# Performance work log

Hardware: AMD Instinct MI355X
Metric: run time of the kernel (lower is better)

The kernel has to match this reference:

```python
import jax, jax.numpy as jnp
import numpy as np

B, S, D, H = 2, 2048, 1024, 16
DK = D // H

def setup_inputs() -> dict:
    key = jax.random.key(0)
    ks = jax.random.split(key, 12)
    scale = 1.0 / np.sqrt(D)
    return {
        "q": jax.random.normal(ks[0], (B, S, D), jnp.float32),
        "k": jax.random.normal(ks[1], (B, S, D), jnp.float32),
        "v": jax.random.normal(ks[2], (B, S, D), jnp.float32),
        "mask": jax.random.randint(ks[3], (B, 1, S, S), 0, 2, jnp.int32),
        "w_q": jax.random.normal(ks[4], (D, D), jnp.float32) * scale,
        "b_q": jnp.zeros((D,), jnp.float32),
        "w_k": jax.random.normal(ks[5], (D, D), jnp.float32) * scale,
        "b_k": jnp.zeros((D,), jnp.float32),
        "w_v": jax.random.normal(ks[6], (D, D), jnp.float32) * scale,
        "b_v": jnp.zeros((D,), jnp.float32),
        "w_o": jax.random.normal(ks[7], (D, D), jnp.float32) * scale,
        "b_o": jnp.zeros((D,), jnp.float32),
    }

def reference(q, k, v, mask, w_q, b_q, w_k, b_k, w_v, b_v, w_o, b_o):
    # projections (nn.Linear: x @ W^T + b)
    Q = q @ w_q.T + b_q  # [B,S,D]
    K = k @ w_k.T + b_k
    V = v @ w_v.T + b_v
    # split heads -> [B,H,S,DK]
    Q = Q.reshape(B, S, H, DK).transpose(0, 2, 1, 3)
    K = K.reshape(B, S, H, DK).transpose(0, 2, 1, 3)
    V = V.reshape(B, S, H, DK).transpose(0, 2, 1, 3)
    scores = jnp.einsum("bhqd,bhkd->bhqk", Q, K) / jnp.sqrt(jnp.float32(DK))
    scores = jnp.where(mask == 0, jnp.float32(-1e9), scores)
    attn = jax.nn.softmax(scores, axis=-1)  # dropout p=0 -> identity
    x = jnp.einsum("bhqk,bhkd->bhqd", attn, V)
    x = x.transpose(0, 2, 1, 3).reshape(B, S, D)
    return x @ w_o.T + b_o
```

## Files before the change

kernel.cpp:

```cpp
#include <hip/hip_runtime.h>
#include <hip/hip_bf16.h>
#include <cstdint>
#include <cstddef>

typedef short bf16x8 __attribute__((ext_vector_type(8)));
typedef short bf16x4v __attribute__((ext_vector_type(4)));
typedef float f32x4 __attribute__((ext_vector_type(4)));
typedef unsigned int uint32x2 __attribute__((ext_vector_type(2)));
typedef __hip_bfloat16 bf16;

constexpr int Bb = 2, Ss = 2048, Dd = 1024, Hh = 16, DKk = 64;

__device__ __forceinline__ void async_lds16(void* lds, const void* g) {
  __builtin_amdgcn_global_load_lds(
      (const __attribute__((address_space(1))) void*)g,
      (__attribute__((address_space(3))) void*)lds, 16, 0, 0);
}

__device__ __forceinline__ float bf2f(bf16 x) { return __bfloat162float(x); }
__device__ __forceinline__ short f2bf(float x) {
  bf16 h = __float2bfloat16(x);
  return *(short*)&h;
}
__device__ __forceinline__ short f2bf_fast(float x) {
  return (short)((__float_as_uint(x) + 0x8000u) >> 16);
}
__device__ __forceinline__ float bfs2f(short s) {
  return __uint_as_float(((uint32_t)(uint16_t)s) << 16);
}
__device__ __forceinline__ uint32_t cvtpk_bf16(float lo, float hi) {
  uint32_t r;
  asm("v_cvt_pk_bf16_f32 %0, %1, %2" : "=v"(r) : "v"(lo), "v"(hi));
  return r;
}
__device__ __forceinline__ uint32x2 pl32swap(uint32_t d, uint32_t s) {
  return __builtin_amdgcn_permlane32_swap(d, s, false, false);
}
__device__ __forceinline__ uint32x2 pl16swap(uint32_t d, uint32_t s) {
  return __builtin_amdgcn_permlane16_swap(d, s, false, false);
}

struct CvtArgs {
  const float* src[12];
  short* dst[12];
  int n[12];
  int count;
};

__global__ __launch_bounds__(256)
void cvt_all(CvtArgs a, const int* __restrict__ mask, uint32_t* __restrict__ bits)
{
  const int t = blockIdx.y;
  if (t == 11) {
    const int stride = 1024 * 256;
    int i = blockIdx.x * 256 + threadIdx.x;
#pragma unroll 4
    for (int it = 0; it < 32; ++it, i += stride) {
      const unsigned long long bal = __ballot(mask[i] != 0);
      if ((threadIdx.x & 63) == 0)
        *(unsigned long long*)(bits + (i >> 5)) = bal;
    }
    return;
  }
  if (t >= a.count) return;
  const float* s = a.src[t];
  short* d = a.dst[t];
  const int n = a.n[t];
  const int stride = gridDim.x * blockDim.x * 4;
  for (int i = (blockIdx.x * blockDim.x + threadIdx.x) * 4; i < n; i += stride) {
    const float4 v = *(const float4*)(s + i);
    bf16x4v o;
    o[0] = f2bf(v.x); o[1] = f2bf(v.y); o[2] = f2bf(v.z); o[3] = f2bf(v.w);
    *(bf16x4v*)(d + i) = o;
  }
}

__global__ __launch_bounds__(256, 3)
void gemm_bt(const bf16* __restrict__ A0, const bf16* __restrict__ A1, const bf16* __restrict__ A2,
             const bf16* __restrict__ W0, const bf16* __restrict__ W1, const bf16* __restrict__ W2,
             const bf16* __restrict__ b0, const bf16* __restrict__ b1, const bf16* __restrict__ b2,
             void* __restrict__ O0, void* __restrict__ O1, void* __restrict__ O2,
             float scale0, int vtrans)
{
  extern __shared__ char smem[];
  const int mt  = blockIdx.x;
  const int by  = blockIdx.y;
  const int mat = by >> 3;
  const int nt  = by & 7;
  const bf16* A    = (mat == 0) ? A0 : (mat == 1) ? A1 : A2;
  const bf16* W    = (mat == 0) ? W0 : (mat == 1) ? W1 : W2;
  const bf16* bias = (mat == 0) ? b0 : (mat == 1) ? b1 : b2;
  void*       Out  = (mat == 0) ? O0 : (mat == 1) ? O1 : O2;
  const float scale = (mat == 0) ? scale0 : 1.0f;

  const int tid  = threadIdx.x;
  const int w    = tid >> 6;
  const int lane = tid & 63;
  const int quad = lane >> 4;
  const int l16  = lane & 15;
  const int wm   = (w & 1) * 64;
  const int wn   = (w >> 1) * 64;

  const int srow = lane >> 3;
  const int sseg = (lane & 7) ^ srow;

  const char* Abytes = (const char*)A;
  const char* Wbytes = (const char*)W;

  f32x4 acc[4][4];
#pragma unroll
  for (int i = 0; i < 4; ++i)
#pragma unroll
    for (int j = 0; j < 4; ++j) acc[i][j] = f32x4{0.f, 0.f, 0.f, 0.f};

  for (int kt = 0; kt < 16; ++kt) {
    __syncthreads();
#pragma unroll
    for (int c = 0; c < 4; ++c) {
      const int r0 = w * 32 + c * 8;
      async_lds16(smem + r0 * 128,
                  Abytes + (size_t)(mt * 128 + r0 + srow) * 2048 + kt * 128 + sseg * 16);
      async_lds16(smem + 16384 + r0 * 128,
                  Wbytes + (size_t)(nt * 128 + r0 + srow) * 2048 + kt * 128 + sseg * 16);
    }
    __syncthreads();
#pragma unroll
    for (int s = 0; s < 2; ++s) {
      bf16x8 af[4], bfg[4];
#pragma unroll
      for (int mb = 0; mb < 4; ++mb) {
        const int row = wm + mb * 16 + l16;
        af[mb] = *(const bf16x8*)(smem + row * 128 + (((4 * s + quad) ^ (row & 7)) * 16));
      }
#pragma unroll
      for (int nb = 0; nb < 4; ++nb) {
        const int row = wn + nb * 16 + l16;
        bfg[nb] = *(const bf16x8*)(smem + 16384 + row * 128 + (((4 * s + quad) ^ (row & 7)) * 16));
      }
#pragma unroll
      for (int mb = 0; mb < 4; ++mb)
#pragma unroll
        for (int nb = 0; nb < 4; ++nb)
          acc[mb][nb] = __builtin_amdgcn_mfma_f32_16x16x32_bf16(af[mb], bfg[nb], acc[mb][nb], 0, 0, 0);
    }
  }

  if (vtrans && mat == 2) {
    __syncthreads();
#pragma unroll
    for (int nb = 0; nb < 4; ++nb) {
      const int dk = wn + nb * 16 + l16;
      const float bv = bf2f(bias[nt * 128 + dk]);
#pragma unroll
      for (int mb = 0; mb < 4; ++mb) {
        const int s0 = wm + mb * 16 + quad * 4;
        bf16x4v pk;
#pragma unroll
        for (int r = 0; r < 4; ++r) pk[r] = f2bf_fast(acc[mb][nb][r] + bv);
        *(bf16x4v*)(smem + dk * 256 + (((s0 >> 3) ^ (dk & 15)) * 16) + (s0 & 7) * 2) = pk;
      }
    }
    __syncthreads();
    const int bidx  = (mt * 128) >> 11;
    const int sbase = (mt * 128) & 2047;
#pragma unroll
    for (int i = 0; i < 8; ++i) {
      const int dk  = i * 16 + (tid >> 4);
      const int seg = tid & 15;
      bf16x8 vrow = *(const bf16x8*)(smem + dk * 256 + ((seg ^ (dk & 15)) * 16));
      *(bf16x8*)((bf16*)Out + (size_t)bidx * 2097152 + (size_t)(nt * 128 + dk) * 2048
                 + sbase + seg * 8) = vrow;
    }
  } else {
#pragma unroll
    for (int nb = 0; nb < 4; ++nb) {
      const int col = nt * 128 + wn + nb * 16 + l16;
      const float bv = bf2f(bias[col]);
#pragma unroll
      for (int mb = 0; mb < 4; ++mb) {
#pragma unroll
        for (int r = 0; r < 4; ++r) {
          const int row = mt * 128 + wm + mb * 16 + quad * 4 + r;
          short s = f2bf_fast((acc[mb][nb][r] + bv) * scale);
          ((short*)Out)[(size_t)row * 1024 + col] = s;
        }
      }
    }
  }
}

__global__ __launch_bounds__(256, 4)
void gemm_out(const bf16* __restrict__ A, const bf16* __restrict__ W,
              const bf16* __restrict__ bias, float* __restrict__ Out)
{
  __shared__ char smem[16384];
  const int mt = blockIdx.x;
  const int nt = blockIdx.y;
  const int tid = threadIdx.x, w = tid >> 6, lane = tid & 63;
  const int quad = lane >> 4, l16 = lane & 15;
  const int wm = (w & 1) * 32, wn = (w >> 1) * 32;
  const int srow = lane >> 3;
  const int sseg = (lane & 7) ^ (srow & 7);

  const char* Abytes = (const char*)A;
  const char* Wbytes = (const char*)W;

  f32x4 acc[2][2];
#pragma unroll
  for (int i = 0; i < 2; ++i)
#pragma unroll
    for (int j = 0; j < 2; ++j) acc[i][j] = f32x4{0.f, 0.f, 0.f, 0.f};

  for (int kt = 0; kt < 16; ++kt) {
    __syncthreads();
#pragma unroll
    for (int c = 0; c < 2; ++c) {
      const int r0 = c * 32 + w * 8;
      async_lds16(smem + c * 4096 + w * 1024,
                  Abytes + (size_t)(mt * 64 + r0 + srow) * 2048 + kt * 128 + sseg * 16);
      async_lds16(smem + 8192 + c * 4096 + w * 1024,
                  Wbytes + (size_t)(nt * 64 + r0 + srow) * 2048 + kt * 128 + sseg * 16);
    }
    __syncthreads();
#pragma unroll
    for (int s = 0; s < 2; ++s) {
      bf16x8 af[2], bfg[2];
#pragma unroll
      for (int mb = 0; mb < 2; ++mb) {
        const int row = wm + mb * 16 + l16;
        af[mb] = *(const bf16x8*)(smem + row * 128 + (((4 * s + quad) ^ (row & 7)) * 16));
      }
#pragma unroll
      for (int nb = 0; nb < 2; ++nb) {
        const int row = wn + nb * 16 + l16;
        bfg[nb] = *(const bf16x8*)(smem + 8192 + row * 128 + (((4 * s + quad) ^ (row & 7)) * 16));
      }
#pragma unroll
      for (int mb = 0; mb < 2; ++mb)
#pragma unroll
        for (int nb = 0; nb < 2; ++nb)
          acc[mb][nb] = __builtin_amdgcn_mfma_f32_16x16x32_bf16(af[mb], bfg[nb], acc[mb][nb], 0, 0, 0);
    }
  }

#pragma unroll
  for (int nb = 0; nb < 2; ++nb) {
    const int col = nt * 64 + wn + nb * 16 + l16;
    const float bv = bf2f(bias[col]);
#pragma unroll
    for (int mb = 0; mb < 2; ++mb) {
#pragma unroll
      for (int r = 0; r < 4; ++r) {
        const int row = mt * 64 + wm + mb * 16 + quad * 4 + r;
        Out[(size_t)row * 1024 + col] = acc[mb][nb][r] + bv;
      }
    }
  }
}

__device__ __forceinline__ void stage_kv(char* KbB, char* VtB,
    const bf16* __restrict__ Kp, const bf16* __restrict__ VpT,
    size_t headoff, size_t vbase, int kb, int w, int lane)
{
#pragma unroll
  for (int c = 0; c < 2; ++c) {
    const int rowK = c * 32 + w * 8 + (lane >> 3);
    const int segK = (lane & 7) ^ (rowK & 7);
    async_lds16(KbB + c * 4096 + w * 1024,
                Kp + headoff + (size_t)(kb + rowK) * Dd + segK * 8);
    const int rowV = c * 32 + w * 8 + (lane >> 3);
    const int segV = (lane & 7) ^ (rowV & 7);
    async_lds16(VtB + c * 4096 + w * 1024,
                VpT + vbase + (size_t)rowV * 2048 + kb + segV * 8);
  }
}

__global__ __launch_bounds__(256, 4)
void attn(const bf16* __restrict__ Qp, const bf16* __restrict__ Kp,
          const bf16* __restrict__ VpT, const uint32_t* __restrict__ mbits,
          bf16* __restrict__ Opart, float* __restrict__ Lpart)
{
  __shared__ char smem[16384];
  char* Kb = smem;
  char* Vt = smem + 8192;

  const int tile  = blockIdx.x;
  const int split = blockIdx.y;
  const int qt = tile & 15, h = (tile >> 4) & 15, b = tile >> 8;
  const int tid = threadIdx.x, w = tid >> 6, lane = tid & 63;
  const int quad = lane >> 4, l16 = lane & 15;
  const int qb = qt * 128;
  const size_t headoff = (size_t)b * (Ss * Dd) + h * DKk;
  const size_t vbase = (size_t)b * 2097152 + (size_t)h * 131072;

  const int kc0 = (split == 0) ? 0 : (split == 1) ? 11 : 22;
  const int kc1 = (split == 0) ? 11 : (split == 1) ? 22 : 32;

  bf16x8 qf[2][2];
#pragma unroll
  for (int set = 0; set < 2; ++set)
#pragma unroll
    for (int s2 = 0; s2 < 2; ++s2) {
      const int row = qb + w * 32 + set * 16 + l16;
      qf[set][s2] = *(const bf16x8*)(Qp + headoff + (size_t)row * Dd + s2 * 32 + quad * 8);
    }

  bf16x8 onesv;
#pragma unroll
  for (int j = 0; j < 8; ++j) onesv[j] = (short)0x3F80;

  f32x4 o[2][4];
  f32x4 oL[2];
#pragma unroll
  for (int set = 0; set < 2; ++set) {
    oL[set] = f32x4{0.f, 0.f, 0.f, 0.f};
#pragma unroll
    for (int nbk = 0; nbk < 4; ++nbk) o[set][nbk] = f32x4{0.f, 0.f, 0.f, 0.f};
  }

  const uint32_t* mrow0 = mbits + (size_t)(b * Ss + qb + w * 32 + l16) * 64;
  const uint32_t* mrow1 = mrow0 + 16 * 64;

  for (int kc = kc0; kc < kc1; ++kc) {
    const int kb = kc * 64;
    const uint2 mwv0 = *(const uint2*)(mrow0 + kc * 2);
    const uint2 mwv1 = *(const uint2*)(mrow1 + kc * 2);
    __syncthreads();
    stage_kv(Kb, Vt, Kp, VpT, headoff, vbase, kb, w, lane);
    __syncthreads();

    const uint32_t mw0[2] = {mwv0.x, mwv0.y};
    const uint32_t mw1[2] = {mwv1.x, mwv1.y};

#pragma unroll
    for (int sl = 0; sl < 2; ++sl) {
      f32x4 sc[2][2];
#pragma unroll
      for (int set = 0; set < 2; ++set)
#pragma unroll
        for (int nbh = 0; nbh < 2; ++nbh) sc[set][nbh] = f32x4{0.f, 0.f, 0.f, 0.f};
      __builtin_amdgcn_s_setprio(1);
#pragma unroll
      for (int s2 = 0; s2 < 2; ++s2)
#pragma unroll
        for (int nbh = 0; nbh < 2; ++nbh) {
          const int row = (sl * 2 + nbh) * 16 + l16;
          bf16x8 kf = *(const bf16x8*)(Kb + row * 128 + (((s2 * 4 + quad) ^ (row & 7)) * 16));
          sc[0][nbh] = __builtin_amdgcn_mfma_f32_16x16x32_bf16(kf, qf[0][s2], sc[0][nbh], 0, 0, 0);
          sc[1][nbh] = __builtin_amdgcn_mfma_f32_16x16x32_bf16(kf, qf[1][s2], sc[1][nbh], 0, 0, 0);
        }
      __builtin_amdgcn_s_setprio(0);

      bf16x8 pf[2];
#pragma unroll
      for (int set = 0; set < 2; ++set) {
        const uint32_t mword = (set == 0) ? mw0[sl] : mw1[sl];
        uint32_t pk[2][2];
#pragma unroll
        for (int nbh = 0; nbh < 2; ++nbh) {
          const uint32_t nib = (mword >> (nbh * 16 + quad * 4)) & 0xFu;
          const float e0 = __builtin_amdgcn_exp2f(sc[set][nbh][0]);
          const float e1 = __builtin_amdgcn_exp2f(sc[set][nbh][1]);
          const float e2 = __builtin_amdgcn_exp2f(sc[set][nbh][2]);
          const float e3 = __builtin_amdgcn_exp2f(sc[set][nbh][3]);
          const float p0 = (nib & 1u) ? e0 : 0.f;
          const float p1 = (nib & 2u) ? e1 : 0.f;
          const float p2 = (nib & 4u) ? e2 : 0.f;
          const float p3 = (nib & 8u) ? e3 : 0.f;
          pk[nbh][0] = cvtpk_bf16(p0, p1);
          pk[nbh][1] = cvtpk_bf16(p2, p3);
        }
        const uint32x2 r0 = pl32swap(pk[0][0], pk[1][0]);
        const uint32x2 r1 = pl32swap(pk[0][1], pk[1][1]);
        const uint32x2 t0 = pl16swap(r0.x, r0.y);
        const uint32x2 t1 = pl16swap(r1.x, r1.y);
        union { uint32_t u[4]; bf16x8 v; } U;
        U.u[0] = t0.x; U.u[1] = t1.x; U.u[2] = t0.y; U.u[3] = t1.y;
        pf[set] = U.v;
      }

      __builtin_amdgcn_s_setprio(1);
      oL[0] = __builtin_amdgcn_mfma_f32_16x16x32_bf16(pf[0], onesv, oL[0], 0, 0, 0);
      oL[1] = __builtin_amdgcn_mfma_f32_16x16x32_bf16(pf[1], onesv, oL[1], 0, 0, 0);
#pragma unroll
      for (int nbk = 0; nbk < 4; ++nbk) {
        const int row = nbk * 16 + l16;
        bf16x8 vf = *(const bf16x8*)(Vt + row * 128 + (((sl * 4 + quad) ^ (row & 7)) * 16));
        o[0][nbk] = __builtin_amdgcn_mfma_f32_16x16x32_bf16(pf[0], vf, o[0][nbk], 0, 0, 0);
        o[1][nbk] = __builtin_amdgcn_mfma_f32_16x16x32_bf16(pf[1], vf, o[1][nbk], 0, 0, 0);
      }
      __builtin_amdgcn_s_setprio(0);
    }
  }

#pragma unroll
  for (int set = 0; set < 2; ++set) {
    const int rbase = tile * 128 + w * 32 + set * 16;
#pragma unroll
    for (int r = 0; r < 4; ++r) {
      const int rglob = rbase + quad * 4 + r;
#pragma unroll
      for (int nbk = 0; nbk < 4; ++nbk) {
        short s = f2bf_fast(o[set][nbk][r]);
        ((short*)Opart)[((size_t)split * 65536 + rglob) * 64 + nbk * 16 + l16] = s;
      }
    }
    if (l16 == 0) {
#pragma unroll
      for (int r = 0; r < 4; ++r)
        Lpart[(size_t)split * 65536 + rbase + quad * 4 + r] = oL[set][r];
    }
  }
}

__global__ __launch_bounds__(256)
void combine(const bf16* __restrict__ Opart, const float* __restrict__ Lpart,
             bf16* __restrict__ Xa)
{
  const int t = threadIdx.x;
  const int row = blockIdx.x * 32 + (t >> 3);
  const int dkc = (t & 7) * 8;
  const float L = Lpart[row] + Lpart[65536 + row] + Lpart[131072 + row];
  const float inv = 1.0f / L;
  const bf16x8 O0 = *(const bf16x8*)(Opart + (size_t)row * 64 + dkc);
  const bf16x8 O1 = *(const bf16x8*)(Opart + ((size_t)65536 + row) * 64 + dkc);
  const bf16x8 O2 = *(const bf16x8*)(Opart + ((size_t)131072 + row) * 64 + dkc);
  bf16x8 res;
#pragma unroll
  for (int j = 0; j < 8; ++j)
    res[j] = f2bf_fast((bfs2f(O0[j]) + bfs2f(O1[j]) + bfs2f(O2[j])) * inv);
  const int tile = row >> 7, qlocal = row & 127;
  const int b = tile >> 8, h = (tile >> 4) & 15, q = (tile & 15) * 128 + qlocal;
  *(bf16x8*)(Xa + (size_t)(b * 2048 + q) * 1024 + h * 64 + dkc) = res;
}

extern "C" void kernel_launch(void* const* d_in, const int* in_sizes, int n_in,
                              void* d_out, int out_size, void* d_ws, size_t ws_size,
                              hipStream_t stream)
{
  const float* q  = (const float*)d_in[0];
  const float* k  = (const float*)d_in[1];
  const float* v  = (const float*)d_in[2];
  const int*   mk = (const int*)d_in[3];
  const float* wq = (const float*)d_in[4];
  const float* bq = (const float*)d_in[5];
  const float* wk = (const float*)d_in[6];
  const float* bk = (const float*)d_in[7];
  const float* wv = (const float*)d_in[8];
  const float* bv = (const float*)d_in[9];
  const float* wo = (const float*)d_in[10];
  const float* bo = (const float*)d_in[11];
  float* out = (float*)d_out;

  char* ws = (char*)d_ws;
  bf16* qb_  = (bf16*)(ws + ((size_t)0  << 20));
  bf16* kb_  = (bf16*)(ws + ((size_t)8  << 20));
  bf16* vb_  = (bf16*)(ws + ((size_t)16 << 20));
  bf16* Qp   = (bf16*)(ws + ((size_t)24 << 20));
  bf16* Kp   = (bf16*)(ws + ((size_t)32 << 20));
  bf16* VpT  = (bf16*)(ws + ((size_t)40 << 20));
  bf16* wqb  = (bf16*)(ws + ((size_t)48 << 20));
  bf16* wkb  = (bf16*)(ws + ((size_t)50 << 20));
  bf16* wvb  = (bf16*)(ws + ((size_t)52 << 20));
  bf16* wob  = (bf16*)(ws + ((size_t)54 << 20));
  bf16* bqb  = (bf16*)(ws + ((size_t)56 << 20));
  bf16* bkb  = (bf16*)(ws + ((size_t)56 << 20) + 2048);
  bf16* bvb  = (bf16*)(ws + ((size_t)56 << 20) + 4096);
  bf16* bob  = (bf16*)(ws + ((size_t)56 << 20) + 6144);
  uint32_t* mbits = (uint32_t*)(ws + ((size_t)56 << 20) + 65536);
  bf16*  Opart = (bf16*)(ws + ((size_t)0 << 20));
  float* Lpart = (float*)(ws + ((size_t)48 << 20));
  bf16*  Xa    = (bf16*)(ws + ((size_t)24 << 20));

  const int NA = Bb * Ss * Dd;
  const int NW = Dd * Dd;

  CvtArgs ca;
  ca.src[0] = q;  ca.dst[0] = (short*)qb_; ca.n[0] = NA;
  ca.src[1] = k;  ca.dst[1] = (short*)kb_; ca.n[1] = NA;
  ca.src[2] = v;  ca.dst[2] = (short*)vb_; ca.n[2] = NA;
  ca.src[3] = wq; ca.dst[3] = (short*)wqb; ca.n[3] = NW;
  ca.src[4] = wk; ca.dst[4] = (short*)wkb; ca.n[4] = NW;
  ca.src[5] = wv; ca.dst[5] = (short*)wvb; ca.n[5] = NW;
  ca.src[6] = wo; ca.dst[6] = (short*)wob; ca.n[6] = NW;
  ca.src[7] = bq; ca.dst[7] = (short*)bqb; ca.n[7] = Dd;
  ca.src[8] = bk; ca.dst[8] = (short*)bkb; ca.n[8] = Dd;
  ca.src[9] = bv; ca.dst[9] = (short*)bvb; ca.n[9] = Dd;
  ca.src[10] = bo; ca.dst[10] = (short*)bob; ca.n[10] = Dd;
  ca.src[11] = bo; ca.dst[11] = (short*)bob; ca.n[11] = 0;
  ca.count = 11;

  dim3 blk(256);
  cvt_all<<<dim3(1024, 12), blk, 0, stream>>>(ca, mk, mbits);

  gemm_bt<<<dim3(32, 24), blk, 32768, stream>>>(qb_, kb_, vb_, wqb, wkb, wvb,
                                                bqb, bkb, bvb,
                                                (void*)Qp, (void*)Kp, (void*)VpT,
                                                0.125f * 1.44269504088896340736f, 1);
  attn<<<dim3(512, 3), blk, 0, stream>>>(Qp, Kp, VpT, mbits, Opart, Lpart);
  combine<<<dim3(2048), blk, 0, stream>>>(Opart, Lpart, Xa);
  gemm_out<<<dim3(64, 16), blk, 0, stream>>>(Xa, wob, bob, out);
}
```

Baseline: 260.7 us.

## Double-buffer K/V tiles in LDS to overlap global loads with MFMA

Adds a second LDS buffer so the next K/V chunk and mask words are prefetched with async global-to-LDS loads while the current chunk is computed. Explicit vmcnt waits and raw barriers replace the two __syncthreads per iteration. This hides load latency behind compute, but doubles shared memory to 32KB per block, which may reduce occupancy under the 4-block launch bound, and relies on a hand-counted vmcnt value of 6.

```diff
diff --git a/kernel.cpp b/kernel.cpp
--- a/kernel.cpp
+++ b/kernel.cpp
@@ -280,9 +280,7 @@
           const bf16* __restrict__ VpT, const uint32_t* __restrict__ mbits,
           bf16* __restrict__ Opart, float* __restrict__ Lpart)
 {
-  __shared__ char smem[16384];
-  char* Kb = smem;
-  char* Vt = smem + 8192;
+  __shared__ char smem[32768];
 
   const int tile  = blockIdx.x;
   const int split = blockIdx.y;
@@ -321,16 +319,29 @@
   const uint32_t* mrow0 = mbits + (size_t)(b * Ss + qb + w * 32 + l16) * 64;
   const uint32_t* mrow1 = mrow0 + 16 * 64;
 
+  char* bufC = smem;
+  char* bufN = smem + 16384;
+  uint2 mc0 = *(const uint2*)(mrow0 + kc0 * 2);
+  uint2 mc1 = *(const uint2*)(mrow1 + kc0 * 2);
+  stage_kv(bufC, bufC + 8192, Kp, VpT, headoff, vbase, kc0 * 64, w, lane);
+
   for (int kc = kc0; kc < kc1; ++kc) {
-    const int kb = kc * 64;
-    const uint2 mwv0 = *(const uint2*)(mrow0 + kc * 2);
-    const uint2 mwv1 = *(const uint2*)(mrow1 + kc * 2);
-    __syncthreads();
-    stage_kv(Kb, Vt, Kp, VpT, headoff, vbase, kb, w, lane);
-    __syncthreads();
-
-    const uint32_t mw0[2] = {mwv0.x, mwv0.y};
-    const uint32_t mw1[2] = {mwv1.x, mwv1.y};
+    uint2 mn0 = mc0, mn1 = mc1;
+    if (kc + 1 < kc1) {
+      mn0 = *(const uint2*)(mrow0 + (kc + 1) * 2);
+      mn1 = *(const uint2*)(mrow1 + (kc + 1) * 2);
+      stage_kv(bufN, bufN + 8192, Kp, VpT, headoff, vbase, (kc + 1) * 64, w, lane);
+      asm volatile("s_waitcnt vmcnt(6)" ::: "memory");
+    } else {
+      asm volatile("s_waitcnt vmcnt(0)" ::: "memory");
+    }
+    __builtin_amdgcn_s_barrier();
+    __builtin_amdgcn_sched_barrier(0);
+
+    char* Kb = bufC;
+    char* Vt = bufC + 8192;
+    const uint32_t mw0[2] = {mc0.x, mc0.y};
+    const uint32_t mw1[2] = {mc1.x, mc1.y};
 
 #pragma unroll
     for (int sl = 0; sl < 2; ++sl) {
@@ -391,6 +402,12 @@
       }
       __builtin_amdgcn_s_setprio(0);
     }
+
+    asm volatile("" ::: "memory");
+    __builtin_amdgcn_s_barrier();
+
+    char* tp = bufC; bufC = bufN; bufN = tp;
+    mc0 = mn0; mc1 = mn1;
   }
 
 #pragma unroll
```

After: 267.3 us. 1.03x slower.
